# Optimization experiments

Hardware: AMD Instinct MI355X
Metric: run time of the kernel (lower is better)

## Reference

```python
import jax, jax.numpy as jnp
import numpy as np

H = 1024

def setup_inputs() -> dict:
    key = jax.random.key(0)
    ks = jax.random.split(key, 9)
    s = 1.0 / np.sqrt(H)
    x = jax.random.normal(ks[0], (4, 2048, H), dtype=jnp.float32)
    Wq = jax.random.uniform(ks[1], (H, H), jnp.float32, -s, s)
    bq = jax.random.uniform(ks[2], (H,), jnp.float32, -s, s)
    Wk = jax.random.uniform(ks[3], (H, H), jnp.float32, -s, s)
    bk = jax.random.uniform(ks[4], (H,), jnp.float32, -s, s)
    Wv = jax.random.uniform(ks[5], (H, H), jnp.float32, -s, s)
    bv = jax.random.uniform(ks[6], (H,), jnp.float32, -s, s)
    Wo = jax.random.uniform(ks[7], (H, H), jnp.float32, -s, s)
    bo = jax.random.uniform(ks[8], (H,), jnp.float32, -s, s)
    return {"x": x, "Wq": Wq, "bq": bq, "Wk": Wk, "bk": bk,
            "Wv": Wv, "bv": bv, "Wo": Wo, "bo": bo}

def reference(x, Wq, bq, Wk, bk, Wv, bv, Wo, bo):
    # Linear uses y = x @ W.T + b (torch convention: W is [out, in])
    q = jnp.einsum('bsd,ed->bse', x, Wq) + bq
    k = jnp.einsum('bsd,ed->bse', x, Wk) + bk
    v = jnp.einsum('bsd,ed->bse', x, Wv) + bv
    scale = q.shape[-1] ** 0.5
    attn = jnp.einsum('bqe,bke->bqk', q, k) / scale  # [B,S,S]
    attn = jax.nn.softmax(attn, axis=-1)
    out = jnp.einsum('bqk,bke->bqe', attn, v)
    return jnp.einsum('bse,oe->bso', out, Wo) + bo
```

## Files before the change

kernel.cpp:

```cpp
#include <hip/hip_runtime.h>

typedef short  short4v __attribute__((ext_vector_type(4)));
typedef short  short8v __attribute__((ext_vector_type(8)));
typedef __bf16 bf16x8  __attribute__((ext_vector_type(8)));
typedef float  f32x4   __attribute__((ext_vector_type(4)));
typedef float  float4v __attribute__((ext_vector_type(4)));

__device__ __forceinline__ short f2bf(float f) {
  unsigned u = __builtin_bit_cast(unsigned, f);
  u += 0x7fffu + ((u >> 16) & 1u);
  return (short)(u >> 16);
}
__device__ __forceinline__ float bf2f(short h) {
  unsigned u = ((unsigned)(unsigned short)h) << 16;
  return __builtin_bit_cast(float, u);
}
__device__ __forceinline__ bf16x8 ld8(const short* p) {
  return __builtin_bit_cast(bf16x8, *reinterpret_cast<const short8v*>(p));
}

__global__ __launch_bounds__(256) void k_cvt(const float* __restrict__ in,
                                             short* __restrict__ out, int n4) {
  int i = blockIdx.x * 256 + threadIdx.x;
  if (i >= n4) return;
  float4v v = *reinterpret_cast<const float4v*>(in + (long)i * 4);
  short4v o;
  o[0] = f2bf(v[0]); o[1] = f2bf(v[1]); o[2] = f2bf(v[2]); o[3] = f2bf(v[3]);
  *reinterpret_cast<short4v*>(out + (long)i * 4) = o;
}

__global__ __launch_bounds__(256) void k_cvtw(const float* __restrict__ w0,
    const float* __restrict__ w1, const float* __restrict__ w2,
    short* __restrict__ o0, short* __restrict__ o1, short* __restrict__ o2) {
  const float* in = blockIdx.y == 0 ? w0 : blockIdx.y == 1 ? w1 : w2;
  short* out = blockIdx.y == 0 ? o0 : blockIdx.y == 1 ? o1 : o2;
  int i = blockIdx.x * 256 + threadIdx.x;
  float4v v = *reinterpret_cast<const float4v*>(in + (long)i * 4);
  short4v o;
  o[0] = f2bf(v[0]); o[1] = f2bf(v[1]); o[2] = f2bf(v[2]); o[3] = f2bf(v[3]);
  *reinterpret_cast<short4v*>(out + (long)i * 4) = o;
}

__global__ __launch_bounds__(256) void k_cvtT(const float* __restrict__ in,
                                              short* __restrict__ out) {
  __shared__ float tile[16][17];
  const int lx = threadIdx.x & 15, ly = threadIdx.x >> 4;
  const int bx = blockIdx.x << 4, by = blockIdx.y << 4;
  tile[ly][lx] = in[(long)(by + ly) * 1024 + bx + lx];
  __syncthreads();
  out[(long)(bx + ly) * 1024 + by + lx] = f2bf(tile[lx][ly]);
}

__global__ __launch_bounds__(256) void k_matvec(const float* __restrict__ W,
    const float* __restrict__ v, float* __restrict__ o) {
  const int row = blockIdx.x * 4 + (threadIdx.x >> 6), lane = threadIdx.x & 63;
  float s = 0.f;
#pragma unroll
  for (int j = 0; j < 16; ++j)
    s += W[(long)row * 1024 + j * 64 + lane] * v[j * 64 + lane];
#pragma unroll
  for (int off = 32; off; off >>= 1) s += __shfl_xor(s, off);
  if (lane == 0) o[row] = s;
}

template <int MODE>
__global__ __launch_bounds__(256, 3) void k_gemm(
    const short* __restrict__ A, const short* __restrict__ B,
    const float* __restrict__ b0p, const float* __restrict__ b1p,
    const float* __restrict__ b2p,
    void* __restrict__ C0, void* __restrict__ C1, void* __restrict__ C2,
    int K, long sA, long sB, long sC, int ldC) {
  __shared__ __align__(16) short lsA[128 * 64];
  __shared__ __align__(16) short lsB[128 * 64];
  const int tid = threadIdx.x;
  const int lane = tid & 63;
  const int wid = tid >> 6;
  const int wr = wid >> 1, wc = wid & 1;
  const int fr = lane & 15, fq = lane >> 4;
  const int bm = blockIdx.x * 128, bn = blockIdx.y * 128;
  const short* Ab = A + (long)blockIdx.z * sA;
  const short* Bb = B + (long)blockIdx.z * sB;

  f32x4 acc[4][4] = {};

  for (int kt = 0; kt < K; kt += 64) {
    __syncthreads();
#pragma unroll
    for (int c = 0; c < 4; ++c) {
      int idx = c * 256 + tid;
      int row = idx >> 3;
      int colh = (idx & 7) << 3;
      const short* ga = Ab + (long)(bm + row) * K + kt + colh;
      const short* gb = Bb + (long)(bn + row) * K + kt + colh;
      __builtin_amdgcn_global_load_lds(
          (const __attribute__((address_space(1))) void*)ga,
          (__attribute__((address_space(3))) void*)&lsA[(long)idx * 8], 16, 0, 0);
      __builtin_amdgcn_global_load_lds(
          (const __attribute__((address_space(1))) void*)gb,
          (__attribute__((address_space(3))) void*)&lsB[(long)idx * 8], 16, 0, 0);
    }
    __syncthreads();
#pragma unroll
    for (int ks = 0; ks < 64; ks += 32) {
      bf16x8 a[4], b[4];
#pragma unroll
      for (int m = 0; m < 4; ++m)
        a[m] = ld8(&lsA[(wr * 64 + m * 16 + fr) * 64 + ks + fq * 8]);
#pragma unroll
      for (int n = 0; n < 4; ++n)
        b[n] = ld8(&lsB[(wc * 64 + n * 16 + fr) * 64 + ks + fq * 8]);
#pragma unroll
      for (int m = 0; m < 4; ++m)
#pragma unroll
        for (int n = 0; n < 4; ++n)
          acc[m][n] = __builtin_amdgcn_mfma_f32_16x16x32_bf16(a[m], b[n], acc[m][n], 0, 0, 0);
    }
  }

#pragma unroll
  for (int n = 0; n < 4; ++n) {
    const int coll = wc * 64 + n * 16 + fr;
#pragma unroll
    for (int m = 0; m < 4; ++m) {
      const int row0 = bm + wr * 64 + m * 16 + fq * 4;
#pragma unroll
      for (int i = 0; i < 4; ++i) {
        const float vacc = acc[m][n][i];
        if constexpr (MODE == 0) {
          short* O = (short*)C0 + (long)blockIdx.z * sC;
          O[(long)(row0 + i) * ldC + bn + coll] = f2bf(vacc);
        } else if constexpr (MODE == 1) {
          float* O = (float*)C0 + (long)blockIdx.z * sC;
          O[(long)(row0 + i) * ldC + bn + coll] = vacc + b0p[bn + coll];
        } else {
          const int sel = (bn + coll) >> 10;
          const int cl = (bn + coll) & 1023;
          const float bv = (sel == 0 ? b0p : sel == 1 ? b1p : b2p)[cl];
          const float v = vacc + bv;
          const int r = row0 + i;
          if (sel == 0) {
            ((short*)C0)[(long)r * 1024 + cl] = f2bf(v);
          } else if (sel == 1) {
            ((short*)C1)[(long)r * 1024 + cl] = f2bf(v);
          } else {
            const int b = r >> 11, s = r & 2047;
            ((short*)C2)[((long)b << 21) + ((long)cl << 11) + s] = f2bf(v);
          }
        }
      }
    }
  }
}

__global__ __launch_bounds__(256) void k_softmax(short* __restrict__ S) {
  const long base = (long)blockIdx.x * 2048;
  const int t = threadIdx.x, lane = t & 63, wid = t >> 6;
  short8v raw = *reinterpret_cast<const short8v*>(S + base + t * 8);
  float x[8];
#pragma unroll
  for (int j = 0; j < 8; ++j) x[j] = bf2f(raw[j]) * 0.03125f;
  float m = x[0];
#pragma unroll
  for (int j = 1; j < 8; ++j) m = fmaxf(m, x[j]);
#pragma unroll
  for (int off = 32; off; off >>= 1) m = fmaxf(m, __shfl_xor(m, off));
  __shared__ float rmax[4], rsum[4];
  if (lane == 0) rmax[wid] = m;
  __syncthreads();
  m = fmaxf(fmaxf(rmax[0], rmax[1]), fmaxf(rmax[2], rmax[3]));
  float e[8], s = 0.f;
#pragma unroll
  for (int j = 0; j < 8; ++j) { e[j] = __expf(x[j] - m); s += e[j]; }
#pragma unroll
  for (int off = 32; off; off >>= 1) s += __shfl_xor(s, off);
  if (lane == 0) rsum[wid] = s;
  __syncthreads();
  s = rsum[0] + rsum[1] + rsum[2] + rsum[3];
  float inv = 1.0f / s;
  short8v o;
#pragma unroll
  for (int j = 0; j < 8; ++j) o[j] = f2bf(e[j] * inv);
  *reinterpret_cast<short8v*>(S + base + t * 8) = o;
}

extern "C" void kernel_launch(void* const* d_in, const int* in_sizes, int n_in,
                              void* d_out, int out_size, void* d_ws, size_t ws_size,
                              hipStream_t stream) {
  const float* x  = (const float*)d_in[0];
  const float* Wq = (const float*)d_in[1];
  const float* bq = (const float*)d_in[2];
  const float* Wk = (const float*)d_in[3];
  const float* bk = (const float*)d_in[4];
  const float* Wv = (const float*)d_in[5];
  const float* bv = (const float*)d_in[6];
  const float* Wo = (const float*)d_in[7];
  const float* bo = (const float*)d_in[8];

  char* ws = (char*)d_ws;
  short* xb    = (short*)ws; ws += 8192L * 1024 * 2;
  short* wqkvb = (short*)ws; ws += 3072L * 1024 * 2;
  short* wob   = (short*)ws; ws += 1024L * 1024 * 2;
  short* wvT   = (short*)ws; ws += 1024L * 1024 * 2;
  short* qb    = (short*)ws; ws += 8192L * 1024 * 2;
  short* kb    = (short*)ws; ws += 8192L * 1024 * 2;
  short* vT    = (short*)ws; ws += 8192L * 1024 * 2;
  short* Sc    = (short*)ws; ws += 4L * 2048 * 2048 * 2;
  float* bvp   = (float*)ws; ws += 1024L * 4;

  dim3 b256(256);
  k_cvt<<<8192, b256, 0, stream>>>(x, xb, 2097152);
  k_cvtw<<<dim3(1024, 3, 1), b256, 0, stream>>>(
      Wq, Wk, Wo, wqkvb, wqkvb + 1024L * 1024, wob);
  k_cvtT<<<dim3(64, 64, 1), b256, 0, stream>>>(Wv, wvT);
  k_gemm<0><<<dim3(8, 8, 1), b256, 0, stream>>>(
      wob, wvT, nullptr, nullptr, nullptr, wqkvb + 2048L * 1024, nullptr, nullptr,
      1024, 0, 0, 0, 1024);
  k_matvec<<<256, b256, 0, stream>>>(Wo, bv, bvp);

  k_gemm<2><<<dim3(64, 24, 1), b256, 0, stream>>>(
      xb, wqkvb, bq, bk, bvp, qb, kb, vT, 1024, 0, 0, 0, 0);
  k_gemm<0><<<dim3(16, 16, 4), b256, 0, stream>>>(
      qb, kb, nullptr, nullptr, nullptr, Sc, nullptr, nullptr,
      1024, 2048L * 1024, 2048L * 1024, 2048L * 2048, 2048);
  k_softmax<<<8192, b256, 0, stream>>>(Sc);
  k_gemm<1><<<dim3(16, 8, 4), b256, 0, stream>>>(
      Sc, vT, bo, nullptr, nullptr, (float*)d_out, nullptr, nullptr,
      2048, 2048L * 2048, 1024L * 2048, 2048L * 1024, 1024);
}
```

Before: 232.5 us.

## Fuse softmax into score/PV GEMM epilogues and double-buffer GEMM LDS tiles

Removes the separate softmax kernel. The QK^T GEMM epilogue writes exp(score/32) and per-tile row partial sums, and the PV GEMM normalizes rows by the reciprocal of those sums in its epilogue. The GEMM main loop now double-buffers LDS tiles so the next tile's global loads overlap the current MFMAs, with occupancy hint lowered to 2. Q/K are computed as one concatenated output, and V^T is computed by a separate GEMM with a row bias. Skipping max subtraction risks exp overflow for large scores.

```diff
diff --git a/kernel.cpp b/kernel.cpp
--- a/kernel.cpp
+++ b/kernel.cpp
@@ -10,10 +10,6 @@
   unsigned u = __builtin_bit_cast(unsigned, f);
   u += 0x7fffu + ((u >> 16) & 1u);
   return (short)(u >> 16);
-}
-__device__ __forceinline__ float bf2f(short h) {
-  unsigned u = ((unsigned)(unsigned short)h) << 16;
-  return __builtin_bit_cast(float, u);
 }
 __device__ __forceinline__ bf16x8 ld8(const short* p) {
   return __builtin_bit_cast(bf16x8, *reinterpret_cast<const short8v*>(p));
@@ -63,124 +59,127 @@
   if (lane == 0) o[row] = s;
 }
 
+__global__ __launch_bounds__(256) void k_bcat(const float* __restrict__ a,
+    const float* __restrict__ b, float* __restrict__ o) {
+  int i = blockIdx.x * 256 + threadIdx.x;
+  o[i] = i < 1024 ? a[i] : b[i - 1024];
+}
+
 template <int MODE>
-__global__ __launch_bounds__(256, 3) void k_gemm(
+__global__ __launch_bounds__(256, 2) void k_gemm(
     const short* __restrict__ A, const short* __restrict__ B,
-    const float* __restrict__ b0p, const float* __restrict__ b1p,
-    const float* __restrict__ b2p,
-    void* __restrict__ C0, void* __restrict__ C1, void* __restrict__ C2,
-    int K, long sA, long sB, long sC, int ldC) {
-  __shared__ __align__(16) short lsA[128 * 64];
-  __shared__ __align__(16) short lsB[128 * 64];
+    const float* __restrict__ b0p, float* __restrict__ b1p,
+    void* __restrict__ C0,
+    int K, int lda, int ldb, long sA, long sB, long sC, int ldC) {
+  __shared__ __align__(16) short lsA[2][8192];
+  __shared__ __align__(16) short lsB[2][8192];
+  __shared__ float invL[128];
   const int tid = threadIdx.x;
-  const int lane = tid & 63;
-  const int wid = tid >> 6;
+  const int lane = tid & 63, wid = tid >> 6;
   const int wr = wid >> 1, wc = wid & 1;
   const int fr = lane & 15, fq = lane >> 4;
   const int bm = blockIdx.x * 128, bn = blockIdx.y * 128;
   const short* Ab = A + (long)blockIdx.z * sA;
   const short* Bb = B + (long)blockIdx.z * sB;
-
-  f32x4 acc[4][4] = {};
-
-  for (int kt = 0; kt < K; kt += 64) {
-    __syncthreads();
+  const int nt = K >> 6;
+
+  if constexpr (MODE == 4) {
+    if (tid < 128) {
+      const float* pr = b1p + ((long)blockIdx.z * 2048 + bm + tid) * 32;
+      float s = 0.f;
+#pragma unroll
+      for (int j = 0; j < 32; ++j) s += pr[j];
+      invL[tid] = 1.0f / s;
+    }
+  }
+
+  auto stage = [&](int kt, int buf) {
 #pragma unroll
     for (int c = 0; c < 4; ++c) {
-      int idx = c * 256 + tid;
-      int row = idx >> 3;
-      int colh = (idx & 7) << 3;
-      const short* ga = Ab + (long)(bm + row) * K + kt + colh;
-      const short* gb = Bb + (long)(bn + row) * K + kt + colh;
+      const int idx = c * 256 + tid;
+      const int row = idx >> 3, colh = (idx & 7) << 3;
+      const short* ga = Ab + (long)(bm + row) * lda + kt + colh;
+      const short* gb = Bb + (long)(bn + row) * ldb + kt + colh;
       __builtin_amdgcn_global_load_lds(
           (const __attribute__((address_space(1))) void*)ga,
-          (__attribute__((address_space(3))) void*)&lsA[(long)idx * 8], 16, 0, 0);
+          (__attribute__((address_space(3))) void*)&lsA[buf][idx * 8], 16, 0, 0);
       __builtin_amdgcn_global_load_lds(
           (const __attribute__((address_space(1))) void*)gb,
-          (__attribute__((address_space(3))) void*)&lsB[(long)idx * 8], 16, 0, 0);
-    }
-    __syncthreads();
+          (__attribute__((address_space(3))) void*)&lsB[buf][idx * 8], 16, 0, 0);
+    }
+  };
+
+  f32x4 acc[4][4] = {};
+
+  stage(0, 0);
+  __syncthreads();
+  for (int t = 0; t < nt; ++t) {
+    if (t + 1 < nt) stage((t + 1) << 6, (t + 1) & 1);
+    const short* cA = lsA[t & 1];
+    const short* cB = lsB[t & 1];
 #pragma unroll
     for (int ks = 0; ks < 64; ks += 32) {
       bf16x8 a[4], b[4];
 #pragma unroll
       for (int m = 0; m < 4; ++m)
-        a[m] = ld8(&lsA[(wr * 64 + m * 16 + fr) * 64 + ks + fq * 8]);
+        a[m] = ld8(&cA[(wr * 64 + m * 16 + fr) * 64 + ks + fq * 8]);
 #pragma unroll
       for (int n = 0; n < 4; ++n)
-        b[n] = ld8(&lsB[(wc * 64 + n * 16 + fr) * 64 + ks + fq * 8]);
+        b[n] = ld8(&cB[(wc * 64 + n * 16 + fr) * 64 + ks + fq * 8]);
 #pragma unroll
       for (int m = 0; m < 4; ++m)
 #pragma unroll
         for (int n = 0; n < 4; ++n)
           acc[m][n] = __builtin_amdgcn_mfma_f32_16x16x32_bf16(a[m], b[n], acc[m][n], 0, 0, 0);
     }
+    __syncthreads();
   }
 
-#pragma unroll
-  for (int n = 0; n < 4; ++n) {
-    const int coll = wc * 64 + n * 16 + fr;
+  if constexpr (MODE == 3) {
+    short* O = (short*)C0 + (long)blockIdx.z * sC;
 #pragma unroll
     for (int m = 0; m < 4; ++m) {
-      const int row0 = bm + wr * 64 + m * 16 + fq * 4;
 #pragma unroll
       for (int i = 0; i < 4; ++i) {
-        const float vacc = acc[m][n][i];
-        if constexpr (MODE == 0) {
-          short* O = (short*)C0 + (long)blockIdx.z * sC;
-          O[(long)(row0 + i) * ldC + bn + coll] = f2bf(vacc);
-        } else if constexpr (MODE == 1) {
-          float* O = (float*)C0 + (long)blockIdx.z * sC;
-          O[(long)(row0 + i) * ldC + bn + coll] = vacc + b0p[bn + coll];
-        } else {
-          const int sel = (bn + coll) >> 10;
-          const int cl = (bn + coll) & 1023;
-          const float bv = (sel == 0 ? b0p : sel == 1 ? b1p : b2p)[cl];
-          const float v = vacc + bv;
-          const int r = row0 + i;
-          if (sel == 0) {
-            ((short*)C0)[(long)r * 1024 + cl] = f2bf(v);
-          } else if (sel == 1) {
-            ((short*)C1)[(long)r * 1024 + cl] = f2bf(v);
+        const int row = bm + wr * 64 + m * 16 + fq * 4 + i;
+        float rs = 0.f;
+#pragma unroll
+        for (int n = 0; n < 4; ++n) {
+          float e = __expf(acc[m][n][i] * 0.03125f);
+          O[(long)row * ldC + bn + wc * 64 + n * 16 + fr] = f2bf(e);
+          rs += e;
+        }
+        rs += __shfl_xor(rs, 1); rs += __shfl_xor(rs, 2);
+        rs += __shfl_xor(rs, 4); rs += __shfl_xor(rs, 8);
+        if (fr == 0)
+          b1p[((long)blockIdx.z * 2048 + row) * 32 + (blockIdx.y << 1) + wc] = rs;
+      }
+    }
+  } else {
+#pragma unroll
+    for (int n = 0; n < 4; ++n) {
+      const int coll = wc * 64 + n * 16 + fr;
+#pragma unroll
+      for (int m = 0; m < 4; ++m) {
+        const int rl0 = wr * 64 + m * 16 + fq * 4;
+#pragma unroll
+        for (int i = 0; i < 4; ++i) {
+          const float vacc = acc[m][n][i];
+          const long row = bm + rl0 + i, col = bn + coll;
+          if constexpr (MODE == 0) {
+            ((short*)C0)[row * ldC + col] = f2bf(vacc);
+          } else if constexpr (MODE == 2) {
+            ((short*)C0)[row * ldC + col] = f2bf(vacc + b0p[col]);
+          } else if constexpr (MODE == 5) {
+            ((short*)C0)[row * ldC + col] = f2bf(vacc + b0p[row]);
           } else {
-            const int b = r >> 11, s = r & 2047;
-            ((short*)C2)[((long)b << 21) + ((long)cl << 11) + s] = f2bf(v);
+            float* O = (float*)C0 + (long)blockIdx.z * sC;
+            O[row * ldC + col] = vacc * invL[rl0 + i] + b0p[col];
           }
         }
       }
     }
   }
-}
-
-__global__ __launch_bounds__(256) void k_softmax(short* __restrict__ S) {
-  const long base = (long)blockIdx.x * 2048;
-  const int t = threadIdx.x, lane = t & 63, wid = t >> 6;
-  short8v raw = *reinterpret_cast<const short8v*>(S + base + t * 8);
-  float x[8];
-#pragma unroll
-  for (int j = 0; j < 8; ++j) x[j] = bf2f(raw[j]) * 0.03125f;
-  float m = x[0];
-#pragma unroll
-  for (int j = 1; j < 8; ++j) m = fmaxf(m, x[j]);
-#pragma unroll
-  for (int off = 32; off; off >>= 1) m = fmaxf(m, __shfl_xor(m, off));
-  __shared__ float rmax[4], rsum[4];
-  if (lane == 0) rmax[wid] = m;
-  __syncthreads();
-  m = fmaxf(fmaxf(rmax[0], rmax[1]), fmaxf(rmax[2], rmax[3]));
-  float e[8], s = 0.f;
-#pragma unroll
-  for (int j = 0; j < 8; ++j) { e[j] = __expf(x[j] - m); s += e[j]; }
-#pragma unroll
-  for (int off = 32; off; off >>= 1) s += __shfl_xor(s, off);
-  if (lane == 0) rsum[wid] = s;
-  __syncthreads();
-  s = rsum[0] + rsum[1] + rsum[2] + rsum[3];
-  float inv = 1.0f / s;
-  short8v o;
-#pragma unroll
-  for (int j = 0; j < 8; ++j) o[j] = f2bf(e[j] * inv);
-  *reinterpret_cast<short8v*>(S + base + t * 8) = o;
 }
 
 extern "C" void kernel_launch(void* const* d_in, const int* in_sizes, int n_in,
@@ -197,33 +196,36 @@
   const float* bo = (const float*)d_in[8];
 
   char* ws = (char*)d_ws;
-  short* xb    = (short*)ws; ws += 8192L * 1024 * 2;
-  short* wqkvb = (short*)ws; ws += 3072L * 1024 * 2;
-  short* wob   = (short*)ws; ws += 1024L * 1024 * 2;
-  short* wvT   = (short*)ws; ws += 1024L * 1024 * 2;
-  short* qb    = (short*)ws; ws += 8192L * 1024 * 2;
-  short* kb    = (short*)ws; ws += 8192L * 1024 * 2;
-  short* vT    = (short*)ws; ws += 8192L * 1024 * 2;
-  short* Sc    = (short*)ws; ws += 4L * 2048 * 2048 * 2;
-  float* bvp   = (float*)ws; ws += 1024L * 4;
+  short* xb   = (short*)ws; ws += 8192L * 1024 * 2;
+  short* wqkb = (short*)ws; ws += 2048L * 1024 * 2;
+  short* wob  = (short*)ws; ws += 1024L * 1024 * 2;
+  short* wvT  = (short*)ws; ws += 1024L * 1024 * 2;
+  short* wv2b = (short*)ws; ws += 1024L * 1024 * 2;
+  short* qkb  = (short*)ws; ws += 8192L * 2048 * 2;
+  short* vTp  = (short*)ws; ws += 1024L * 8192 * 2;
+  short* Sc   = (short*)ws; ws += 4L * 2048 * 2048 * 2;
+  float* psum = (float*)ws; ws += 4L * 2048 * 32 * 4;
+  float* bqk  = (float*)ws; ws += 2048L * 4;
+  float* bvp  = (float*)ws; ws += 1024L * 4;
 
   dim3 b256(256);
   k_cvt<<<8192, b256, 0, stream>>>(x, xb, 2097152);
   k_cvtw<<<dim3(1024, 3, 1), b256, 0, stream>>>(
-      Wq, Wk, Wo, wqkvb, wqkvb + 1024L * 1024, wob);
+      Wq, Wk, Wo, wqkb, wqkb + 1024L * 1024, wob);
   k_cvtT<<<dim3(64, 64, 1), b256, 0, stream>>>(Wv, wvT);
+  k_bcat<<<8, b256, 0, stream>>>(bq, bk, bqk);
+  k_matvec<<<256, b256, 0, stream>>>(Wo, bv, bvp);
+
   k_gemm<0><<<dim3(8, 8, 1), b256, 0, stream>>>(
-      wob, wvT, nullptr, nullptr, nullptr, wqkvb + 2048L * 1024, nullptr, nullptr,
-      1024, 0, 0, 0, 1024);
-  k_matvec<<<256, b256, 0, stream>>>(Wo, bv, bvp);
-
-  k_gemm<2><<<dim3(64, 24, 1), b256, 0, stream>>>(
-      xb, wqkvb, bq, bk, bvp, qb, kb, vT, 1024, 0, 0, 0, 0);
-  k_gemm<0><<<dim3(16, 16, 4), b256, 0, stream>>>(
-      qb, kb, nullptr, nullptr, nullptr, Sc, nullptr, nullptr,
-      1024, 2048L * 1024, 2048L * 1024, 2048L * 2048, 2048);
-  k_softmax<<<8192, b256, 0, stream>>>(Sc);
-  k_gemm<1><<<dim3(16, 8, 4), b256, 0, stream>>>(
-      Sc, vT, bo, nullptr, nullptr, (float*)d_out, nullptr, nullptr,
-      2048, 2048L * 2048, 1024L * 2048, 2048L * 1024, 1024);
-}
+      wob, wvT, nullptr, nullptr, wv2b, 1024, 1024, 1024, 0, 0, 0, 1024);
+  k_gemm<2><<<dim3(64, 16, 1), b256, 0, stream>>>(
+      xb, wqkb, bqk, nullptr, qkb, 1024, 1024, 1024, 0, 0, 0, 2048);
+  k_gemm<5><<<dim3(8, 64, 1), b256, 0, stream>>>(
+      wv2b, xb, bvp, nullptr, vTp, 1024, 1024, 1024, 0, 0, 0, 8192);
+  k_gemm<3><<<dim3(16, 16, 4), b256, 0, stream>>>(
+      qkb, qkb + 1024, nullptr, psum, Sc,
+      1024, 2048, 2048, 2048L * 2048, 2048L * 2048, 2048L * 2048, 2048);
+  k_gemm<4><<<dim3(16, 8, 4), b256, 0, stream>>>(
+      Sc, vTp, bo, psum, (float*)d_out,
+      2048, 2048, 8192, 2048L * 2048, 2048, 2048L * 1024, 1024);
+}
```

Result: no change. 236.0 us (+1.5%).
